# Kernel optimization log

Hardware: AMD Instinct MI355X
Metric: run time of the kernel (lower is better)

Reference implementation:

```python
import jax, jax.numpy as jnp
import numpy as np

N_NODES = 100000
N_EDGES = 1600000
IN_CH = 128
HEADS = 4
OUT_CH = 32
NEG_SLOPE = 0.2
EPS = 1e-10


def setup_inputs() -> dict:
    key = jax.random.key(0)
    k1, k2, k3, k4 = jax.random.split(key, 4)
    x = jax.random.normal(k1, (N_NODES, IN_CH), dtype=jnp.float32)
    edge_index = jax.random.randint(k2, (2, N_EDGES), 0, N_NODES, dtype=jnp.int64)
    # small scale keeps exp(-leakyrelu(score)) numerically tame
    W = jax.random.normal(k3, (IN_CH, HEADS * OUT_CH), dtype=jnp.float32) * 0.05
    attention = jax.random.normal(k4, (HEADS, 2 * OUT_CH), dtype=jnp.float32) * 0.05
    bias = jnp.zeros((HEADS * OUT_CH,), dtype=jnp.float32)
    return {"x": x, "edge_index": edge_index, "W": W, "attention": attention, "bias": bias}


def reference(x, edge_index, W, attention, bias):
    N = x.shape[0]
    H, two_o = attention.shape
    O = two_o // 2
    # shared fc_src == fc_tgt (in_channels is an int in the original)
    h = (x @ W).reshape(N, H, O)  # [N, H, O]
    # attention vector splits over the concat [h_src || h_tgt]
    a_src, a_tgt = attention[:, :O], attention[:, O:]
    s_src = jnp.einsum('nho,ho->nh', h, a_src)  # [N, H]
    s_tgt = jnp.einsum('nho,ho->nh', h, a_tgt)  # [N, H]
    src, tgt = edge_index[0], edge_index[1]
    score = s_src[src] + s_tgt[tgt]  # [E, H]
    # NOTE: original applies exp to the NEGATED LeakyReLU output
    e = jnp.exp(-jax.nn.leaky_relu(score, NEG_SLOPE))  # [E, H]
    # numerator: sum_j e_ij * h_src[j] scattered to target nodes
    num = jax.ops.segment_sum(e[:, :, None] * h[src], tgt, num_segments=N)  # [N, H, O]
    den = jax.ops.segment_sum(e, tgt, num_segments=N)  # [N, H]
    out = num / jnp.clip(den, EPS, None)[:, :, None]
    out = out.reshape(N, H * O)  # concat=True
    return out + bias
```

## Files before the change

kernel.cpp:

```cpp
#include <hip/hip_runtime.h>
#include <stdint.h>


#define NN 100000
#define EE 1600000
#define INCH 128
#define HO 128
#define HEADS 4
#define OUTC 32

#define BSH 8
#define NBUCK ((NN + 255) >> BSH)
#define CAPBK 5120
#define CHA 2048
#define ABLK ((EE + CHA - 1) / CHA)

typedef unsigned short ushort_t;
typedef unsigned int uint_t;
typedef __attribute__((ext_vector_type(8))) short bf16x8;
typedef __attribute__((ext_vector_type(4))) float f32x4;

__device__ __forceinline__ float bfl(uint_t u) { return __uint_as_float(u << 16); }
__device__ __forceinline__ float bfh(uint_t u) { return __uint_as_float(u & 0xffff0000u); }
__device__ __forceinline__ uint_t f2bf(float f) {
    uint_t u = __float_as_uint(f);
    u = (u + 0x7fffu + ((u >> 16) & 1u)) >> 16;
    return u;
}

__global__ __launch_bounds__(256) void prepW_k(const float* __restrict__ W,
                                               ushort_t* __restrict__ gWtHi,
                                               ushort_t* __restrict__ gWtLo) {
    const int gidx = blockIdx.x * 256 + threadIdx.x;
    const int col = gidx & 127;
    const int k = gidx >> 7;
    const float v = W[k * 128 + col];
    const uint_t h = f2bf(v);
    const uint_t lo = f2bf(v - bfl(h));
    const int byteOff = (col * 256 + k * 2) ^ ((col & 7) << 4);
    *(ushort_t*)((char*)gWtHi + byteOff) = (ushort_t)h;
    *(ushort_t*)((char*)gWtLo + byteOff) = (ushort_t)lo;
}

__global__ __launch_bounds__(256) void gemm_h(const float* __restrict__ x,
                                              const ushort_t* __restrict__ gWtHi,
                                              const ushort_t* __restrict__ gWtLo,
                                              const float* __restrict__ att,
                                              ushort_t* __restrict__ hb,
                                              float* __restrict__ s_src,
                                              float* __restrict__ s_tgt) {
    __shared__ __align__(16) char smem[81920];
    ushort_t* wtHi = (ushort_t*)smem;
    ushort_t* wtLo = (ushort_t*)(smem + 32768);
    ushort_t* xHi  = (ushort_t*)(smem + 65536);
    ushort_t* xLo  = (ushort_t*)(smem + 73728);
    const int tid = threadIdx.x;
    const int row0 = blockIdx.x * 32;

    {
        const uint4* gh = (const uint4*)gWtHi;
        const uint4* gl = (const uint4*)gWtLo;
        uint4* lh = (uint4*)wtHi;
        uint4* ll = (uint4*)wtLo;
#pragma unroll
        for (int j = 0; j < 8; ++j) lh[tid + 256 * j] = gh[tid + 256 * j];
#pragma unroll
        for (int j = 0; j < 8; ++j) ll[tid + 256 * j] = gl[tid + 256 * j];
    }
    {
        const float4* x4 = (const float4*)(x + (size_t)row0 * INCH);
#pragma unroll
        for (int j = 0; j < 4; ++j) {
            const int i = tid + 256 * j;
            const int row = i >> 5;
            const int k4 = i & 31;
            const float4 v = x4[i];
            const uint_t h0 = f2bf(v.x), h1 = f2bf(v.y), h2 = f2bf(v.z), h3 = f2bf(v.w);
            const uint_t l0 = f2bf(v.x - bfl(h0));
            const uint_t l1 = f2bf(v.y - bfl(h1));
            const uint_t l2 = f2bf(v.z - bfl(h2));
            const uint_t l3 = f2bf(v.w - bfl(h3));
            const int byteOff = (row * 256 + k4 * 8) ^ ((row & 7) << 4);
            *(uint2*)((char*)xHi + byteOff) = make_uint2(h0 | (h1 << 16), h2 | (h3 << 16));
            *(uint2*)((char*)xLo + byteOff) = make_uint2(l0 | (l1 << 16), l2 | (l3 << 16));
        }
    }
    __syncthreads();

    const int lane = tid & 63;
    const int w = tid >> 6;
    const int l15 = lane & 15;
    const int g = lane >> 4;
    const int swz = (l15 & 7) << 4;

    f32x4 acc[2][2] = {};
#pragma unroll
    for (int ks = 0; ks < 4; ++ks) {
        const int kb = ks * 64 + g * 16;
        const bf16x8 a0h = *(const bf16x8*)((char*)xHi + ((l15 * 256 + kb) ^ swz));
        const bf16x8 a1h = *(const bf16x8*)((char*)xHi + (((16 + l15) * 256 + kb) ^ swz));
        const bf16x8 a0l = *(const bf16x8*)((char*)xLo + ((l15 * 256 + kb) ^ swz));
        const bf16x8 a1l = *(const bf16x8*)((char*)xLo + (((16 + l15) * 256 + kb) ^ swz));
        const int c0b = ((w * 32 + l15) * 256 + kb) ^ swz;
        const int c1b = ((w * 32 + 16 + l15) * 256 + kb) ^ swz;
        const bf16x8 b0h = *(const bf16x8*)((char*)wtHi + c0b);
        const bf16x8 b1h = *(const bf16x8*)((char*)wtHi + c1b);
        const bf16x8 b0l = *(const bf16x8*)((char*)wtLo + c0b);
        const bf16x8 b1l = *(const bf16x8*)((char*)wtLo + c1b);
        acc[0][0] = __builtin_amdgcn_mfma_f32_16x16x32_bf16(a0h, b0h, acc[0][0], 0, 0, 0);
        acc[0][1] = __builtin_amdgcn_mfma_f32_16x16x32_bf16(a0h, b1h, acc[0][1], 0, 0, 0);
        acc[1][0] = __builtin_amdgcn_mfma_f32_16x16x32_bf16(a1h, b0h, acc[1][0], 0, 0, 0);
        acc[1][1] = __builtin_amdgcn_mfma_f32_16x16x32_bf16(a1h, b1h, acc[1][1], 0, 0, 0);
        acc[0][0] = __builtin_amdgcn_mfma_f32_16x16x32_bf16(a0h, b0l, acc[0][0], 0, 0, 0);
        acc[0][1] = __builtin_amdgcn_mfma_f32_16x16x32_bf16(a0h, b1l, acc[0][1], 0, 0, 0);
        acc[1][0] = __builtin_amdgcn_mfma_f32_16x16x32_bf16(a1h, b0l, acc[1][0], 0, 0, 0);
        acc[1][1] = __builtin_amdgcn_mfma_f32_16x16x32_bf16(a1h, b1l, acc[1][1], 0, 0, 0);
        acc[0][0] = __builtin_amdgcn_mfma_f32_16x16x32_bf16(a0l, b0h, acc[0][0], 0, 0, 0);
        acc[0][1] = __builtin_amdgcn_mfma_f32_16x16x32_bf16(a0l, b1h, acc[0][1], 0, 0, 0);
        acc[1][0] = __builtin_amdgcn_mfma_f32_16x16x32_bf16(a1l, b0h, acc[1][0], 0, 0, 0);
        acc[1][1] = __builtin_amdgcn_mfma_f32_16x16x32_bf16(a1l, b1h, acc[1][1], 0, 0, 0);
    }

#pragma unroll
    for (int mt = 0; mt < 2; ++mt)
#pragma unroll
        for (int ntl = 0; ntl < 2; ++ntl) {
            const int col = w * 32 + ntl * 16 + l15;
#pragma unroll
            for (int r = 0; r < 4; ++r) {
                const int row = row0 + mt * 16 + g * 4 + r;
                hb[(size_t)row * HO + col] = (ushort_t)f2bf(acc[mt][ntl][r]);
            }
        }

    const float cs0 = att[w * 64 + l15];
    const float cs1 = att[w * 64 + 16 + l15];
    const float ct0 = att[w * 64 + 32 + l15];
    const float ct1 = att[w * 64 + 48 + l15];
#pragma unroll
    for (int mt = 0; mt < 2; ++mt)
#pragma unroll
        for (int r = 0; r < 4; ++r) {
            float ps = acc[mt][0][r] * cs0 + acc[mt][1][r] * cs1;
            float pt = acc[mt][0][r] * ct0 + acc[mt][1][r] * ct1;
#pragma unroll
            for (int d = 1; d < 16; d <<= 1) {
                ps += __shfl_xor(ps, d, 64);
                pt += __shfl_xor(pt, d, 64);
            }
            if (l15 == 0) {
                const int row = row0 + mt * 16 + g * 4 + r;
                s_src[row * 4 + w] = ps;
                s_tgt[row * 4 + w] = pt;
            }
        }
}

__global__ __launch_bounds__(256) void bucketA_k(const int* __restrict__ ei,
                                                 int* __restrict__ gcur,
                                                 uint_t* __restrict__ grec) {
    __shared__ int hist[NBUCK];
    __shared__ int gbase[NBUCK];
    __shared__ int lcur[NBUCK];
    const int tid = threadIdx.x;
    const int e0 = blockIdx.x * CHA;
    const int cnt = min(CHA, EE - e0);

    for (int b = tid; b < NBUCK; b += 256) hist[b] = 0;
    __syncthreads();
    for (int i = tid; i < cnt; i += 256)
        atomicAdd(&hist[ei[EE + e0 + i] >> BSH], 1);
    __syncthreads();
    for (int b = tid; b < NBUCK; b += 256) {
        const int h = hist[b];
        gbase[b] = b * CAPBK + (h ? atomicAdd(&gcur[b], h) : 0);
        lcur[b] = 0;
    }
    __syncthreads();
    for (int i = tid; i < cnt; i += 256) {
        const int src = ei[e0 + i];
        const int tgt = ei[EE + e0 + i];
        const int b = tgt >> BSH;
        const int p = atomicAdd(&lcur[b], 1);
        grec[gbase[b] + p] = (uint_t)src | ((uint_t)(tgt & 255) << 17);
    }
}

__global__ __launch_bounds__(256) void bucketB_k(const int* __restrict__ bucketCnt,
                                                 const uint_t* __restrict__ grec,
                                                 int2* __restrict__ offs2,
                                                 int* __restrict__ sorted_src) {
    __shared__ int cur[256];
    __shared__ int scn[256];
    __shared__ uint_t sbuf[CAPBK];
    const int tid = threadIdx.x;
    const int b = blockIdx.x;
    const int n0 = b << BSH;
    const int nn = min(256, NN - n0);
    const int R0 = b * CAPBK;
    const int cnt = min(bucketCnt[b], CAPBK);

    cur[tid] = 0;
    __syncthreads();
    for (int i = tid; i < cnt; i += 256)
        atomicAdd(&cur[grec[R0 + i] >> 17], 1);
    __syncthreads();
    const int v = cur[tid];
    scn[tid] = v;
    __syncthreads();
#pragma unroll
    for (int off = 1; off < 256; off <<= 1) {
        int u = (tid >= off) ? scn[tid - off] : 0;
        __syncthreads();
        scn[tid] += u;
        __syncthreads();
    }
    const int ex = scn[tid] - v;
    cur[tid] = ex;
    if (tid < nn) offs2[n0 + tid] = make_int2(R0 + ex, R0 + ex + v);
    __syncthreads();
    for (int i = tid; i < cnt; i += 256) {
        const uint_t r = grec[R0 + i];
        const int p = atomicAdd(&cur[r >> 17], 1);
        sbuf[p] = r;
    }
    __syncthreads();
    for (int i = tid; i < cnt; i += 256)
        sorted_src[R0 + i] = (int)(sbuf[i] & 0x1FFFF);
}

__device__ __forceinline__ void gstep(int e, int m, int eg, int hd, int c0,
                                      int srcv, float st,
                                      const float* __restrict__ s_src,
                                      const ushort_t* __restrict__ hb,
                                      float ax[8], float& wsum) {
    const int idx = e + eg;
    const int s = __shfl(srcv, idx, 64);
    float sc = s_src[s * 4 + hd] + st;
    sc = fmaxf(sc, 0.2f * sc);
    float w = __expf(-sc);
    w = (idx < m) ? w : 0.f;
    const uint4 v = *(const uint4*)(hb + (size_t)s * HO + c0);
    ax[0] = fmaf(w, bfl(v.x), ax[0]); ax[1] = fmaf(w, bfh(v.x), ax[1]);
    ax[2] = fmaf(w, bfl(v.y), ax[2]); ax[3] = fmaf(w, bfh(v.y), ax[3]);
    ax[4] = fmaf(w, bfl(v.z), ax[4]); ax[5] = fmaf(w, bfh(v.z), ax[5]);
    ax[6] = fmaf(w, bfl(v.w), ax[6]); ax[7] = fmaf(w, bfh(v.w), ax[7]);
    wsum += w;
}

__global__ __launch_bounds__(256) void gather_k(const int2* __restrict__ offs2,
                                                const int* __restrict__ sorted_src,
                                                const float* __restrict__ s_src,
                                                const float* __restrict__ s_tgt,
                                                const ushort_t* __restrict__ hb,
                                                const float* __restrict__ bias,
                                                float* __restrict__ out) {
    const int n = blockIdx.x * 4 + (threadIdx.x >> 6);
    const int l = threadIdx.x & 63;
    const int eg = l >> 4;
    const int ch16 = l & 15;
    const int hd = ch16 >> 2;
    const int c0 = ch16 * 8;
    const int2 pr = offs2[n];
    const int p0 = pr.x;
    const int deg = pr.y - pr.x;
    const float st = s_tgt[n * 4 + hd];
    float ax[8] = {};
    float wsum = 0.f;
    for (int base = 0; base < deg; base += 64) {
        const int m = min(deg - base, 64);
        const int srcv = sorted_src[p0 + base + ((l < m) ? l : 0)];
        for (int e = 0; e < m; e += 8) {
            gstep(e, m, eg, hd, c0, srcv, st, s_src, hb, ax, wsum);
            gstep(e + 4, m, eg, hd, c0, srcv, st, s_src, hb, ax, wsum);
        }
    }
#pragma unroll
    for (int d = 16; d <= 32; d <<= 1) {
#pragma unroll
        for (int j = 0; j < 8; ++j) ax[j] += __shfl_xor(ax[j], d, 64);
        wsum += __shfl_xor(wsum, d, 64);
    }
    if (eg == 0) {
        const float inv = 1.f / fmaxf(wsum, 1e-10f);
        const float4 b0 = *(const float4*)(bias + c0);
        const float4 b1 = *(const float4*)(bias + c0 + 4);
        float4 o0, o1;
        o0.x = fmaf(ax[0], inv, b0.x); o0.y = fmaf(ax[1], inv, b0.y);
        o0.z = fmaf(ax[2], inv, b0.z); o0.w = fmaf(ax[3], inv, b0.w);
        o1.x = fmaf(ax[4], inv, b1.x); o1.y = fmaf(ax[5], inv, b1.y);
        o1.z = fmaf(ax[6], inv, b1.z); o1.w = fmaf(ax[7], inv, b1.w);
        *(float4*)(out + (size_t)n * HO + c0) = o0;
        *(float4*)(out + (size_t)n * HO + c0 + 4) = o1;
    }
}

extern "C" void kernel_launch(void* const* d_in, const int* in_sizes, int n_in,
                              void* d_out, int out_size, void* d_ws, size_t ws_size,
                              hipStream_t stream) {
    const float* x    = (const float*)d_in[0];
    const int*   ei   = (const int*)d_in[1];
    const float* W    = (const float*)d_in[2];
    const float* att  = (const float*)d_in[3];
    const float* bias = (const float*)d_in[4];
    float* out = (float*)d_out;

    char* ws = (char*)d_ws;
    const size_t HB_B  = (size_t)NN * HO * 2;
    const size_t SS_B  = (size_t)NBUCK * CAPBK * 4;
    const size_t GR_B  = (size_t)NBUCK * CAPBK * 4;
    const size_t S_B   = (size_t)NN * HEADS * 4;
    const size_t OF_B  = ((size_t)NN * 8 + 15) & ~15ull;
    const size_t GC_B  = ((size_t)NBUCK * 4 + 15) & ~15ull;
    const size_t WT_B  = 32768;

    size_t o = 0;
    ushort_t* hb         = (ushort_t*)(ws + o); o += HB_B;
    int*      sorted_src = (int*)(ws + o); o += SS_B;
    uint_t*   grec       = (uint_t*)(ws + o); o += GR_B;
    float*    ssrc       = (float*)(ws + o); o += S_B;
    float*    stgt       = (float*)(ws + o); o += S_B;
    int2*     offs2      = (int2*)(ws + o); o += OF_B;
    int*      gcur       = (int*)(ws + o); o += GC_B;
    ushort_t* gWtHi      = (ushort_t*)(ws + o); o += WT_B;
    ushort_t* gWtLo      = (ushort_t*)(ws + o); o += WT_B;

    (void)hipMemsetAsync(gcur, 0, GC_B, stream);

    prepW_k<<<64, 256, 0, stream>>>(W, gWtHi, gWtLo);
    gemm_h<<<NN / 32, 256, 0, stream>>>(x, gWtHi, gWtLo, att,
                                        hb, ssrc, stgt);
    bucketA_k<<<ABLK, 256, 0, stream>>>(ei, gcur, grec);
    bucketB_k<<<NBUCK, 256, 0, stream>>>(gcur, grec, offs2, sorted_src);
    gather_k<<<NN / 4, 256, 0, stream>>>(offs2, sorted_src, ssrc, stgt,
                                         hb, bias, out);
}
```

Baseline: 256.3 us.

## Hold W fragments in registers, unroll gather by 16, double bucket chunk

The GEMM kernel stops staging the full hi/lo bf16 W matrix in 64KB of shared memory. Each wave now loads its own W fragments from global memory straight into registers, which cuts LDS use from 80KB to 16KB and should allow more resident blocks. The gather loop drops the per-64-edge shuffle broadcast and reads sorted_src directly, processing 16 edges per iteration with clamped indices to expose more memory-level parallelism. The bucket chunk size CHA is also doubled, which halves the number of bucketing blocks. The trade-offs are higher register pressure in the GEMM and redundant sorted_src loads across lanes in the gather.

```diff
diff --git a/kernel.cpp b/kernel.cpp
--- a/kernel.cpp
+++ b/kernel.cpp
@@ -12,7 +12,7 @@
 #define BSH 8
 #define NBUCK ((NN + 255) >> BSH)
 #define CAPBK 5120
-#define CHA 2048
+#define CHA 4096
 #define ABLK ((EE + CHA - 1) / CHA)
 
 typedef unsigned short ushort_t;
@@ -37,9 +37,8 @@
     const float v = W[k * 128 + col];
     const uint_t h = f2bf(v);
     const uint_t lo = f2bf(v - bfl(h));
-    const int byteOff = (col * 256 + k * 2) ^ ((col & 7) << 4);
-    *(ushort_t*)((char*)gWtHi + byteOff) = (ushort_t)h;
-    *(ushort_t*)((char*)gWtLo + byteOff) = (ushort_t)lo;
+    gWtHi[col * 128 + k] = (ushort_t)h;
+    gWtLo[col * 128 + k] = (ushort_t)lo;
 }
 
 __global__ __launch_bounds__(256) void gemm_h(const float* __restrict__ x,
@@ -49,24 +48,31 @@
                                               ushort_t* __restrict__ hb,
                                               float* __restrict__ s_src,
                                               float* __restrict__ s_tgt) {
-    __shared__ __align__(16) char smem[81920];
-    ushort_t* wtHi = (ushort_t*)smem;
-    ushort_t* wtLo = (ushort_t*)(smem + 32768);
-    ushort_t* xHi  = (ushort_t*)(smem + 65536);
-    ushort_t* xLo  = (ushort_t*)(smem + 73728);
+    __shared__ __align__(16) char smem[16384];
+    ushort_t* xHi  = (ushort_t*)smem;
+    ushort_t* xLo  = (ushort_t*)(smem + 8192);
     const int tid = threadIdx.x;
     const int row0 = blockIdx.x * 32;
 
+    const int lane = tid & 63;
+    const int w = tid >> 6;
+    const int l15 = lane & 15;
+    const int g = lane >> 4;
+    const int swz = (l15 & 7) << 4;
+
+    bf16x8 bh[2][4], bl[2][4];
     {
-        const uint4* gh = (const uint4*)gWtHi;
-        const uint4* gl = (const uint4*)gWtLo;
-        uint4* lh = (uint4*)wtHi;
-        uint4* ll = (uint4*)wtLo;
-#pragma unroll
-        for (int j = 0; j < 8; ++j) lh[tid + 256 * j] = gh[tid + 256 * j];
-#pragma unroll
-        for (int j = 0; j < 8; ++j) ll[tid + 256 * j] = gl[tid + 256 * j];
-    }
+        const ushort_t* pH = gWtHi + (size_t)(w * 32 + l15) * 128 + g * 8;
+        const ushort_t* pL = gWtLo + (size_t)(w * 32 + l15) * 128 + g * 8;
+#pragma unroll
+        for (int ntl = 0; ntl < 2; ++ntl)
+#pragma unroll
+            for (int ks = 0; ks < 4; ++ks) {
+                bh[ntl][ks] = *(const bf16x8*)(pH + ntl * 16 * 128 + ks * 32);
+                bl[ntl][ks] = *(const bf16x8*)(pL + ntl * 16 * 128 + ks * 32);
+            }
+    }
+
     {
         const float4* x4 = (const float4*)(x + (size_t)row0 * INCH);
 #pragma unroll
@@ -87,12 +93,6 @@
     }
     __syncthreads();
 
-    const int lane = tid & 63;
-    const int w = tid >> 6;
-    const int l15 = lane & 15;
-    const int g = lane >> 4;
-    const int swz = (l15 & 7) << 4;
-
     f32x4 acc[2][2] = {};
 #pragma unroll
     for (int ks = 0; ks < 4; ++ks) {
@@ -101,24 +101,18 @@
         const bf16x8 a1h = *(const bf16x8*)((char*)xHi + (((16 + l15) * 256 + kb) ^ swz));
         const bf16x8 a0l = *(const bf16x8*)((char*)xLo + ((l15 * 256 + kb) ^ swz));
         const bf16x8 a1l = *(const bf16x8*)((char*)xLo + (((16 + l15) * 256 + kb) ^ swz));
-        const int c0b = ((w * 32 + l15) * 256 + kb) ^ swz;
-        const int c1b = ((w * 32 + 16 + l15) * 256 + kb) ^ swz;
-        const bf16x8 b0h = *(const bf16x8*)((char*)wtHi + c0b);
-        const bf16x8 b1h = *(const bf16x8*)((char*)wtHi + c1b);
-        const bf16x8 b0l = *(const bf16x8*)((char*)wtLo + c0b);
-        const bf16x8 b1l = *(const bf16x8*)((char*)wtLo + c1b);
-        acc[0][0] = __builtin_amdgcn_mfma_f32_16x16x32_bf16(a0h, b0h, acc[0][0], 0, 0, 0);
-        acc[0][1] = __builtin_amdgcn_mfma_f32_16x16x32_bf16(a0h, b1h, acc[0][1], 0, 0, 0);
-        acc[1][0] = __builtin_amdgcn_mfma_f32_16x16x32_bf16(a1h, b0h, acc[1][0], 0, 0, 0);
-        acc[1][1] = __builtin_amdgcn_mfma_f32_16x16x32_bf16(a1h, b1h, acc[1][1], 0, 0, 0);
-        acc[0][0] = __builtin_amdgcn_mfma_f32_16x16x32_bf16(a0h, b0l, acc[0][0], 0, 0, 0);
-        acc[0][1] = __builtin_amdgcn_mfma_f32_16x16x32_bf16(a0h, b1l, acc[0][1], 0, 0, 0);
-        acc[1][0] = __builtin_amdgcn_mfma_f32_16x16x32_bf16(a1h, b0l, acc[1][0], 0, 0, 0);
-        acc[1][1] = __builtin_amdgcn_mfma_f32_16x16x32_bf16(a1h, b1l, acc[1][1], 0, 0, 0);
-        acc[0][0] = __builtin_amdgcn_mfma_f32_16x16x32_bf16(a0l, b0h, acc[0][0], 0, 0, 0);
-        acc[0][1] = __builtin_amdgcn_mfma_f32_16x16x32_bf16(a0l, b1h, acc[0][1], 0, 0, 0);
-        acc[1][0] = __builtin_amdgcn_mfma_f32_16x16x32_bf16(a1l, b0h, acc[1][0], 0, 0, 0);
-        acc[1][1] = __builtin_amdgcn_mfma_f32_16x16x32_bf16(a1l, b1h, acc[1][1], 0, 0, 0);
+        acc[0][0] = __builtin_amdgcn_mfma_f32_16x16x32_bf16(a0h, bh[0][ks], acc[0][0], 0, 0, 0);
+        acc[0][1] = __builtin_amdgcn_mfma_f32_16x16x32_bf16(a0h, bh[1][ks], acc[0][1], 0, 0, 0);
+        acc[1][0] = __builtin_amdgcn_mfma_f32_16x16x32_bf16(a1h, bh[0][ks], acc[1][0], 0, 0, 0);
+        acc[1][1] = __builtin_amdgcn_mfma_f32_16x16x32_bf16(a1h, bh[1][ks], acc[1][1], 0, 0, 0);
+        acc[0][0] = __builtin_amdgcn_mfma_f32_16x16x32_bf16(a0h, bl[0][ks], acc[0][0], 0, 0, 0);
+        acc[0][1] = __builtin_amdgcn_mfma_f32_16x16x32_bf16(a0h, bl[1][ks], acc[0][1], 0, 0, 0);
+        acc[1][0] = __builtin_amdgcn_mfma_f32_16x16x32_bf16(a1h, bl[0][ks], acc[1][0], 0, 0, 0);
+        acc[1][1] = __builtin_amdgcn_mfma_f32_16x16x32_bf16(a1h, bl[1][ks], acc[1][1], 0, 0, 0);
+        acc[0][0] = __builtin_amdgcn_mfma_f32_16x16x32_bf16(a0l, bh[0][ks], acc[0][0], 0, 0, 0);
+        acc[0][1] = __builtin_amdgcn_mfma_f32_16x16x32_bf16(a0l, bh[1][ks], acc[0][1], 0, 0, 0);
+        acc[1][0] = __builtin_amdgcn_mfma_f32_16x16x32_bf16(a1l, bh[0][ks], acc[1][0], 0, 0, 0);
+        acc[1][1] = __builtin_amdgcn_mfma_f32_16x16x32_bf16(a1l, bh[1][ks], acc[1][1], 0, 0, 0);
     }
 
 #pragma unroll
@@ -229,17 +223,17 @@
         sorted_src[R0 + i] = (int)(sbuf[i] & 0x1FFFF);
 }
 
-__device__ __forceinline__ void gstep(int e, int m, int eg, int hd, int c0,
-                                      int srcv, float st,
+__device__ __forceinline__ void gstep(int pe, int plast, int hd, int c0, float st,
+                                      const int* __restrict__ sorted_src,
                                       const float* __restrict__ s_src,
                                       const ushort_t* __restrict__ hb,
                                       float ax[8], float& wsum) {
-    const int idx = e + eg;
-    const int s = __shfl(srcv, idx, 64);
+    const int pc = min(pe, plast);
+    const int s = sorted_src[pc];
     float sc = s_src[s * 4 + hd] + st;
     sc = fmaxf(sc, 0.2f * sc);
     float w = __expf(-sc);
-    w = (idx < m) ? w : 0.f;
+    w = (pe <= plast) ? w : 0.f;
     const uint4 v = *(const uint4*)(hb + (size_t)s * HO + c0);
     ax[0] = fmaf(w, bfl(v.x), ax[0]); ax[1] = fmaf(w, bfh(v.x), ax[1]);
     ax[2] = fmaf(w, bfl(v.y), ax[2]); ax[3] = fmaf(w, bfh(v.y), ax[3]);
@@ -262,18 +256,15 @@
     const int hd = ch16 >> 2;
     const int c0 = ch16 * 8;
     const int2 pr = offs2[n];
-    const int p0 = pr.x;
-    const int deg = pr.y - pr.x;
+    const int pend = pr.y, plast = pr.y - 1;
     const float st = s_tgt[n * 4 + hd];
     float ax[8] = {};
     float wsum = 0.f;
-    for (int base = 0; base < deg; base += 64) {
-        const int m = min(deg - base, 64);
-        const int srcv = sorted_src[p0 + base + ((l < m) ? l : 0)];
-        for (int e = 0; e < m; e += 8) {
-            gstep(e, m, eg, hd, c0, srcv, st, s_src, hb, ax, wsum);
-            gstep(e + 4, m, eg, hd, c0, srcv, st, s_src, hb, ax, wsum);
-        }
+    for (int p = pr.x; p < pend; p += 16) {
+        gstep(p + eg,      plast, hd, c0, st, sorted_src, s_src, hb, ax, wsum);
+        gstep(p + 4 + eg,  plast, hd, c0, st, sorted_src, s_src, hb, ax, wsum);
+        gstep(p + 8 + eg,  plast, hd, c0, st, sorted_src, s_src, hb, ax, wsum);
+        gstep(p + 12 + eg, plast, hd, c0, st, sorted_src, s_src, hb, ax, wsum);
     }
 #pragma unroll
     for (int d = 16; d <= 32; d <<= 1) {
```

Result: no change. 253.1 us (-1.2%).
